# Optimization experiments

Hardware: AMD Instinct MI355X
Metric: run time of the kernel (lower is better)

## Reference

```python
import jax, jax.numpy as jnp
import numpy as np

# Multi-scale feature pyramid (H, W) per level: strides 8/16/32/64 on a ~512px image
SHAPES = ((64, 64), (32, 32), (16, 16), (8, 8))
N_HEADS, N_LEVELS, N_POINTS = 8, 4, 4
D_MODEL = 256
HEAD_DIM = D_MODEL // N_HEADS


def setup_inputs() -> dict:
    key = jax.random.key(0)
    ks = jax.random.split(key, 11)
    B, C = 4, D_MODEL
    Lv = sum(h * w for h, w in SHAPES)  # 5440
    Lq = Lv  # encoder self-attention: queries are the flattened features
    scale = 0.02
    return {
        "query": jax.random.normal(ks[0], (B, Lq, C), jnp.float32),
        "reference_points": jax.random.uniform(ks[1], (B, Lq, N_LEVELS, 2), jnp.float32),
        "value": jax.random.normal(ks[2], (B, Lv, C), jnp.float32),
        "W_off": jax.random.normal(ks[3], (C, N_HEADS * N_LEVELS * N_POINTS * 2), jnp.float32) * scale,
        "b_off": jax.random.normal(ks[4], (N_HEADS * N_LEVELS * N_POINTS * 2,), jnp.float32) * 0.5,
        "W_attn": jax.random.normal(ks[5], (C, N_HEADS * N_LEVELS * N_POINTS), jnp.float32) * scale,
        "b_attn": jax.random.normal(ks[6], (N_HEADS * N_LEVELS * N_POINTS,), jnp.float32) * scale,
        "W_val": jax.random.normal(ks[7], (C, C), jnp.float32) * scale,
        "b_val": jax.random.normal(ks[8], (C,), jnp.float32) * scale,
        "W_out": jax.random.normal(ks[9], (C, C), jnp.float32) * scale,
        "b_out": jax.random.normal(ks[10], (C,), jnp.float32) * scale,
    }


def _bilinear_sample(val, grid, H, W):
    """Replicates F.grid_sample(mode='bilinear', padding_mode='zeros', align_corners=False).

    val:  [N, C, H, W]
    grid: [N, Lq, P, 2] in [-1, 1] (x, y order)
    returns: [N, C, Lq, P]
    """
    N, C = val.shape[0], val.shape[1]
    # unnormalize (align_corners=False)
    x = (grid[..., 0] + 1.0) * 0.5 * W - 0.5  # [N, Lq, P]
    y = (grid[..., 1] + 1.0) * 0.5 * H - 0.5
    x0 = jnp.floor(x)
    y0 = jnp.floor(y)
    wx = x - x0  # fractional parts
    wy = y - y0
    flat = val.reshape(N, C, H * W)

    def gather(xi, yi):
        valid = (xi >= 0) & (xi < W) & (yi >= 0) & (yi < H)
        xc = jnp.clip(xi, 0, W - 1).astype(jnp.int32)
        yc = jnp.clip(yi, 0, H - 1).astype(jnp.int32)
        idx = yc * W + xc  # [N, Lq, P]
        g = jax.vmap(lambda v, i: v[:, i])(flat, idx)  # [N, C, Lq, P]
        return g * valid[:, None, :, :].astype(val.dtype)

    out = (gather(x0, y0) * ((1 - wx) * (1 - wy))[:, None]
           + gather(x0 + 1, y0) * (wx * (1 - wy))[:, None]
           + gather(x0, y0 + 1) * ((1 - wx) * wy)[:, None]
           + gather(x0 + 1, y0 + 1) * (wx * wy)[:, None])
    return out


def _ms_deform_attn(query, reference_points, value, W_off, b_off, W_attn, b_attn,
                    W_val, b_val, W_out, b_out):
    B, Lq, C = query.shape
    val = value @ W_val + b_val  # [B, Lv, C]
    val = val.reshape(B, -1, N_HEADS, HEAD_DIM)

    offsets = (query @ W_off + b_off).reshape(B, Lq, N_HEADS, N_LEVELS, N_POINTS, 2)
    weights = jax.nn.softmax(
        (query @ W_attn + b_attn).reshape(B, Lq, N_HEADS, N_LEVELS * N_POINTS), axis=-1
    ).reshape(B, Lq, N_HEADS, N_LEVELS, N_POINTS)

    # offset normalizer: (W, H) per level
    offset_norm = jnp.array([[w, h] for h, w in SHAPES], jnp.float32)
    # ref_dim == 2 branch
    locs = reference_points[:, :, None, :, None, :] + offsets / offset_norm[None, None, None, :, None, :]
    grids = 2.0 * locs - 1.0  # [B, Lq, nh, nl, np, 2]

    acc = jnp.zeros((B * N_HEADS, HEAD_DIM, Lq), query.dtype)
    start = 0
    for lid, (H, W) in enumerate(SHAPES):
        # [B, HW, nh, hd] -> [B*nh, hd, H, W]
        v = val[:, start:start + H * W].transpose(0, 2, 3, 1).reshape(B * N_HEADS, HEAD_DIM, H, W)
        g = grids[:, :, :, lid].transpose(0, 2, 1, 3, 4).reshape(B * N_HEADS, Lq, N_POINTS, 2)
        s = _bilinear_sample(v, g, H, W)  # [B*nh, hd, Lq, np]
        w = weights[:, :, :, lid].transpose(0, 2, 1, 3).reshape(B * N_HEADS, 1, Lq, N_POINTS)
        acc = acc + (s * w).sum(-1)
        start += H * W

    out = acc.reshape(B, D_MODEL, Lq).transpose(0, 2, 1)  # [B, Lq, C]
    return out @ W_out + b_out


def reference(query, reference_points, value, W_off, b_off, W_attn, b_attn,
              W_val, b_val, W_out, b_out):
    return _ms_deform_attn(query, reference_points, value, W_off, b_off,
                           W_attn, b_attn, W_val, b_val, W_out, b_out)
```

## Files before the change

kernel.cpp:

```cpp
#include <hip/hip_runtime.h>


typedef __attribute__((ext_vector_type(8))) _Float16 half8;
typedef __attribute__((ext_vector_type(4))) _Float16 half4;
typedef __attribute__((ext_vector_type(4))) float f32x4;

typedef __attribute__((address_space(3))) unsigned int lds_uint;
typedef const __attribute__((address_space(1))) unsigned int g_uint;

__device__ __forceinline__ void load_lds16(const _Float16* g, _Float16* l) {
    __builtin_amdgcn_global_load_lds((g_uint*)g, (lds_uint*)l, 16, 0, 0);
}

__device__ __forceinline__ half8 splat8(_Float16 v) {
    half8 r = {v, v, v, v, v, v, v, v};
    return r;
}

#define M_TOTAL 21760

__global__ __launch_bounds__(256) void prep_w(
    const float* __restrict__ W_val, const float* __restrict__ W_off,
    const float* __restrict__ W_attn, _Float16* __restrict__ wtf)
{
    const int slot = blockIdx.x * 256 + threadIdx.x;
    const int T = slot >> 11;
    const int rem = slot & 2047;
    const int n = rem >> 5;
    const int k0 = (rem & 31) * 8;
    half8 h;
#pragma unroll
    for (int e = 0; e < 8; ++e) {
        const int k = k0 + e;
        float v;
        if (T < 4) {
            v = W_val[k * 256 + T * 64 + n];
        } else {
            const int n2 = (T - 4) * 64 + n;
            v = (n2 < 256) ? W_off[k * 256 + n2] : W_attn[k * 128 + (n2 - 256)];
        }
        h[e] = (_Float16)v;
    }
    const int dbyte = T * 32768 + n * 512 + ((k0 * 2) ^ ((n & 7) << 4));
    *(half8*)(wtf + (dbyte >> 1)) = h;
}

__global__ __launch_bounds__(256) void gemm12_cvt(
    const float* __restrict__ value, const float* __restrict__ query,
    const _Float16* __restrict__ wtf,
    const float* __restrict__ b_val, const float* __restrict__ b_off,
    const float* __restrict__ b_attn,
    _Float16* __restrict__ valh, _Float16* __restrict__ offh)
{
    __shared__ _Float16 Asw[64 * 256];
    __shared__ _Float16 Bsw[64 * 256];

    const int bid = ((int)blockIdx.x % 8) * 425 + ((int)blockIdx.x / 8);

    const bool g1 = bid < 1360;
    const int id = g1 ? bid : bid - 1360;
    const int mt = g1 ? (id >> 2) : (id / 6);
    const int nt = g1 ? (id & 3) : (id % 6);
    const int NN = g1 ? 256 : 384;
    const float* A = g1 ? value : query;
    _Float16* C = g1 ? valh : offh;
    const int bm = mt * 64;
    const int bn = nt * 64;
    const int T  = g1 ? nt : 4 + nt;

    const int tid = threadIdx.x;
    const int wave = tid >> 6, lane = tid & 63;
    const int ml = lane & 15, q = lane >> 4;

    const _Float16* wsrc = wtf + ((size_t)T << 14);
#pragma unroll
    for (int i = 0; i < 8; ++i)
        load_lds16(wsrc + (((size_t)i * 256 + tid) << 3),
                   Bsw + (((size_t)i * 256 + wave * 64) << 3));

    const int rbase = wave * 16;
    float4 pa[16];
#pragma unroll
    for (int rr = 0; rr < 16; ++rr)
        pa[rr] = *(const float4*)(A + (size_t)(bm + rbase + rr) * 256 + lane * 4);
#pragma unroll
    for (int rr = 0; rr < 16; ++rr) {
        const int row = rbase + rr;
        const float4 v = pa[rr];
        const half4 h = {(_Float16)v.x, (_Float16)v.y, (_Float16)v.z, (_Float16)v.w};
        const int wbyte = row * 512 + ((lane * 8) ^ ((row & 7) << 4));
        *(half4*)(Asw + (wbyte >> 1)) = h;
    }

    __syncthreads();

    const int swl = (ml & 7) << 4;
    const int abase = (rbase + ml) * 512;

    const f32x4 zero4 = {0.f, 0.f, 0.f, 0.f};
    f32x4 acc[4] = {zero4, zero4, zero4, zero4};

#pragma unroll
    for (int kt = 0; kt < 8; ++kt) {
        const int koff = (kt * 64 + q * 16) ^ swl;
        const half8 af = *(const half8*)(Asw + ((abase + koff) >> 1));
#pragma unroll
        for (int j = 0; j < 4; ++j) {
            const half8 bf = *(const half8*)(Bsw + ((((j * 16 + ml) * 512) + koff) >> 1));
            acc[j] = __builtin_amdgcn_mfma_f32_16x16x32_f16(af, bf, acc[j], 0, 0, 0);
        }
    }

    const int r0 = q * 4;
#pragma unroll
    for (int j = 0; j < 4; ++j) {
        const int col = bn + j * 16 + ml;
        const float bj = g1 ? b_val[col] : (col < 256 ? b_off[col] : b_attn[col - 256]);
        const size_t rbaseC = (size_t)(bm + rbase + r0) * NN + col;
#pragma unroll
        for (int r = 0; r < 4; ++r)
            C[rbaseC + (size_t)r * NN] = (_Float16)(acc[j][r] + bj);
    }
}

__device__ __forceinline__ void gemm_core(
    const _Float16* __restrict__ A, const _Float16* __restrict__ Bt,
    const float* __restrict__ bias, float* __restrict__ Cv,
    int NN, int mt, int nt)
{
    __shared__ _Float16 Ah[128 * 32];
    __shared__ _Float16 Bh[64 * 32];

    const int tid = threadIdx.x;
    const int bm = mt * 128;
    const int bn = nt * 64;
    const int wave = tid >> 6, lane = tid & 63;
    const int wm = (wave & 1) * 64, wn = (wave >> 1) * 32;
    const int ml = lane & 15, kq = (lane >> 4) * 8;
    const int lr = lane >> 2;
    const int lk = (lane & 3) * 8;

    const f32x4 zero4 = {0.f, 0.f, 0.f, 0.f};
    f32x4 acc[4][2];
#pragma unroll
    for (int i = 0; i < 4; ++i)
#pragma unroll
        for (int j = 0; j < 2; ++j) acc[i][j] = zero4;

    for (int kt = 0; kt < 8; ++kt) {
        const int k0 = kt * 32;
        __syncthreads();
#pragma unroll
        for (int t = 0; t < 2; ++t) {
            const int row = wave * 32 + t * 16;
            load_lds16(A + (size_t)(bm + row + lr) * 256 + k0 + lk,
                       Ah + (size_t)row * 32);
        }
        {
            const int row = wave * 16;
            load_lds16(Bt + (size_t)(bn + row + lr) * 256 + k0 + lk,
                       Bh + (size_t)row * 32);
        }
        __syncthreads();

        half8 af[4], bf[2];
#pragma unroll
        for (int i = 0; i < 4; ++i)
            af[i] = *(const half8*)(Ah + (wm + i * 16 + ml) * 32 + kq);
#pragma unroll
        for (int j = 0; j < 2; ++j)
            bf[j] = *(const half8*)(Bh + (wn + j * 16 + ml) * 32 + kq);
#pragma unroll
        for (int i = 0; i < 4; ++i)
#pragma unroll
            for (int j = 0; j < 2; ++j)
                acc[i][j] = __builtin_amdgcn_mfma_f32_16x16x32_f16(af[i], bf[j], acc[i][j], 0, 0, 0);
    }

    const int r0 = (lane >> 4) * 4;
#pragma unroll
    for (int j = 0; j < 2; ++j) {
        const int col = bn + wn + j * 16 + ml;
        const float bj = bias[col];
#pragma unroll
        for (int i = 0; i < 4; ++i) {
            const size_t rbase = (size_t)(bm + wm + i * 16 + r0) * NN + col;
#pragma unroll
            for (int r = 0; r < 4; ++r)
                Cv[rbase + (size_t)r * NN] = acc[i][j][r] + bj;
        }
    }
}

__global__ __launch_bounds__(256) void gemm_single(
    const _Float16* __restrict__ A, const _Float16* __restrict__ Bt,
    const float* __restrict__ bias, float* __restrict__ Cv)
{
    const int id = blockIdx.x;
    gemm_core(A, Bt, bias, Cv, 256, id >> 2, id & 3);
}

__global__ __launch_bounds__(256, 4) void sample_f16(
    const _Float16* __restrict__ valh,
    const float* __restrict__ refp,
    const _Float16* __restrict__ offh,
    const float* __restrict__ W_out,
    _Float16* __restrict__ wto,
    _Float16* __restrict__ acc_out)
{
    if (blockIdx.x < 256)
        wto[blockIdx.x * 256 + threadIdx.x] =
            (_Float16)W_out[threadIdx.x * 256 + blockIdx.x];

    const int wave = threadIdx.x >> 6, lane = threadIdx.x & 63;
    const int q2 = lane >> 5, sl = lane & 31;
    const int bq = blockIdx.x * 8 + wave * 2 + q2;
    const int b = bq / 5440;
    const int h = sl >> 2;
    const int t = sl & 3;
    const int d8 = t * 8;

    const int Wt = 64 >> t;
    const float fW = (float)Wt;

    const half8 ofr = *(const half8*)(offh + (size_t)bq * 384 + h * 32 + t * 8);
    const half4 lgt = *(const half4*)(offh + (size_t)bq * 384 + 256 + h * 16 + t * 4);
    const float2 rxy = *(const float2*)(refp + (size_t)bq * 8 + t * 2);

    float lg[4];
#pragma unroll
    for (int p = 0; p < 4; ++p) lg[p] = (float)lgt[p];

    float mx = fmaxf(fmaxf(lg[0], lg[1]), fmaxf(lg[2], lg[3]));
    mx = fmaxf(mx, __shfl_xor(mx, 1));
    mx = fmaxf(mx, __shfl_xor(mx, 2));
    float s = 0.f;
#pragma unroll
    for (int p = 0; p < 4; ++p) { lg[p] = __expf(lg[p] - mx); s += lg[p]; }
    s += __shfl_xor(s, 1);
    s += __shfl_xor(s, 2);
    const float inv = 1.f / s;

    unsigned pk[16];
#pragma unroll
    for (int p = 0; p < 4; ++p) {
        const float aw = lg[p] * inv;
        const float ox = (float)ofr[p * 2];
        const float oy = (float)ofr[p * 2 + 1];
        const float x = fmaf(rxy.x, fW, ox) - 0.5f;
        const float y = fmaf(rxy.y, fW, oy) - 0.5f;
        const float x0f = floorf(x), y0f = floorf(y);
        const int x0 = (int)x0f, y0 = (int)y0f;
        const float wx = x - x0f, wy = y - y0f;
        const bool okx0 = ((unsigned)x0 < (unsigned)Wt);
        const bool okx1 = ((unsigned)(x0 + 1) < (unsigned)Wt);
        const bool oky0 = ((unsigned)y0 < (unsigned)Wt);
        const bool oky1 = ((unsigned)(y0 + 1) < (unsigned)Wt);
        const int xc0 = min(max(x0, 0), Wt - 1);
        const int xc1 = min(max(x0 + 1, 0), Wt - 1);
        const int yc0 = min(max(y0, 0), Wt - 1);
        const int yc1 = min(max(y0 + 1, 0), Wt - 1);
        const _Float16 w0 = (_Float16)((okx0 & oky0) ? (1.f - wx) * (1.f - wy) * aw : 0.f);
        const _Float16 w1 = (_Float16)((okx1 & oky0) ? wx * (1.f - wy) * aw : 0.f);
        const _Float16 w2 = (_Float16)((okx0 & oky1) ? (1.f - wx) * wy * aw : 0.f);
        const _Float16 w3 = (_Float16)((okx1 & oky1) ? wx * wy * aw : 0.f);
        pk[p * 4 + 0] = ((unsigned)(yc0 * Wt + xc0) << 16) |
                        (unsigned)__builtin_bit_cast(unsigned short, w0);
        pk[p * 4 + 1] = ((unsigned)(yc0 * Wt + xc1) << 16) |
                        (unsigned)__builtin_bit_cast(unsigned short, w1);
        pk[p * 4 + 2] = ((unsigned)(yc1 * Wt + xc0) << 16) |
                        (unsigned)__builtin_bit_cast(unsigned short, w2);
        pk[p * 4 + 3] = ((unsigned)(yc1 * Wt + xc1) << 16) |
                        (unsigned)__builtin_bit_cast(unsigned short, w3);
    }

    const int starts_[4] = {0, 4096, 5120, 5376};
    const int gbase = lane & ~3;

    half8 acc = splat8((_Float16)0.f);
#pragma unroll
    for (int l = 0; l < 4; ++l) {
        const _Float16* vbase = valh + ((size_t)(b * 5440 + starts_[l])) * 256 + h * 32 + d8;
        const int src = gbase + l;

        unsigned q_[16];
#pragma unroll
        for (int c = 0; c < 16; ++c)
            q_[c] = (unsigned)__shfl((int)pk[c], src);

        __builtin_amdgcn_sched_barrier(0);
        half8 c_[16];
#pragma unroll
        for (int c = 0; c < 16; ++c)
            c_[c] = *(const half8*)(vbase + ((size_t)(q_[c] >> 16) << 8));
        __builtin_amdgcn_sched_barrier(0);
#pragma unroll
        for (int c = 0; c < 16; ++c)
            acc += c_[c] * splat8(__builtin_bit_cast(_Float16, (unsigned short)(q_[c] & 0xffffu)));
    }

    *(half8*)(acc_out + (size_t)bq * 256 + h * 32 + d8) = acc;
}

extern "C" void kernel_launch(void* const* d_in, const int* in_sizes, int n_in,
                              void* d_out, int out_size, void* d_ws, size_t ws_size,
                              hipStream_t stream) {
    const float* query  = (const float*)d_in[0];
    const float* refp   = (const float*)d_in[1];
    const float* value  = (const float*)d_in[2];
    const float* W_off  = (const float*)d_in[3];
    const float* b_off  = (const float*)d_in[4];
    const float* W_attn = (const float*)d_in[5];
    const float* b_attn = (const float*)d_in[6];
    const float* W_val  = (const float*)d_in[7];
    const float* b_val  = (const float*)d_in[8];
    const float* W_out  = (const float*)d_in[9];
    const float* b_out  = (const float*)d_in[10];
    float* out = (float*)d_out;

    const size_t M = M_TOTAL;

    _Float16* valh  = (_Float16*)d_ws;
    _Float16* offh  = valh + M * 256;
    _Float16* acc16 = offh + M * 384;
    _Float16* wto   = acc16 + M * 256;
    _Float16* wtf   = wto + 256 * 256;

    dim3 blk(256);
    prep_w<<<dim3(80), blk, 0, stream>>>(W_val, W_off, W_attn, wtf);
    gemm12_cvt<<<dim3(3400), blk, 0, stream>>>(
        value, query, wtf, b_val, b_off, b_attn, valh, offh);
    sample_f16<<<dim3(M / 8), blk, 0, stream>>>(valh, refp, offh, W_out, wto, acc16);
    gemm_single<<<dim3(680), blk, 0, stream>>>(acc16, wto, b_out, out);
}
```

Baseline: 178.9 us.

## Fuse output projection GEMM into sampling kernel via LDS-staged MFMA

The sampling kernel now handles 16 queries per 512-thread block and writes its per-query attention output into a swizzled LDS tile. It then multiplies that tile by the transposed W_out with MFMA and writes the final fp32 output plus bias, so the separate output GEMM launch and the fp16 intermediate round trip through global memory go away. The W_out transpose/convert moves into the prep_w kernel. The cost is that every block rereads the full 256x256 W_out from global or L2 without LDS staging, and the new launch bounds may change occupancy of the gather-heavy sampling phase.

```diff
diff --git a/kernel.cpp b/kernel.cpp
--- a/kernel.cpp
+++ b/kernel.cpp
@@ -21,8 +21,14 @@
 
 __global__ __launch_bounds__(256) void prep_w(
     const float* __restrict__ W_val, const float* __restrict__ W_off,
-    const float* __restrict__ W_attn, _Float16* __restrict__ wtf)
+    const float* __restrict__ W_attn, const float* __restrict__ W_out,
+    _Float16* __restrict__ wtf, _Float16* __restrict__ wto)
 {
+    if (blockIdx.x >= 80) {
+        const int n = blockIdx.x - 80;
+        wto[n * 256 + threadIdx.x] = (_Float16)W_out[threadIdx.x * 256 + n];
+        return;
+    }
     const int slot = blockIdx.x * 256 + threadIdx.x;
     const int T = slot >> 11;
     const int rem = slot & 2047;
@@ -123,98 +129,21 @@
     }
 }
 
-__device__ __forceinline__ void gemm_core(
-    const _Float16* __restrict__ A, const _Float16* __restrict__ Bt,
-    const float* __restrict__ bias, float* __restrict__ Cv,
-    int NN, int mt, int nt)
-{
-    __shared__ _Float16 Ah[128 * 32];
-    __shared__ _Float16 Bh[64 * 32];
-
-    const int tid = threadIdx.x;
-    const int bm = mt * 128;
-    const int bn = nt * 64;
-    const int wave = tid >> 6, lane = tid & 63;
-    const int wm = (wave & 1) * 64, wn = (wave >> 1) * 32;
-    const int ml = lane & 15, kq = (lane >> 4) * 8;
-    const int lr = lane >> 2;
-    const int lk = (lane & 3) * 8;
-
-    const f32x4 zero4 = {0.f, 0.f, 0.f, 0.f};
-    f32x4 acc[4][2];
-#pragma unroll
-    for (int i = 0; i < 4; ++i)
-#pragma unroll
-        for (int j = 0; j < 2; ++j) acc[i][j] = zero4;
-
-    for (int kt = 0; kt < 8; ++kt) {
-        const int k0 = kt * 32;
-        __syncthreads();
-#pragma unroll
-        for (int t = 0; t < 2; ++t) {
-            const int row = wave * 32 + t * 16;
-            load_lds16(A + (size_t)(bm + row + lr) * 256 + k0 + lk,
-                       Ah + (size_t)row * 32);
-        }
-        {
-            const int row = wave * 16;
-            load_lds16(Bt + (size_t)(bn + row + lr) * 256 + k0 + lk,
-                       Bh + (size_t)row * 32);
-        }
-        __syncthreads();
-
-        half8 af[4], bf[2];
-#pragma unroll
-        for (int i = 0; i < 4; ++i)
-            af[i] = *(const half8*)(Ah + (wm + i * 16 + ml) * 32 + kq);
-#pragma unroll
-        for (int j = 0; j < 2; ++j)
-            bf[j] = *(const half8*)(Bh + (wn + j * 16 + ml) * 32 + kq);
-#pragma unroll
-        for (int i = 0; i < 4; ++i)
-#pragma unroll
-            for (int j = 0; j < 2; ++j)
-                acc[i][j] = __builtin_amdgcn_mfma_f32_16x16x32_f16(af[i], bf[j], acc[i][j], 0, 0, 0);
-    }
-
-    const int r0 = (lane >> 4) * 4;
-#pragma unroll
-    for (int j = 0; j < 2; ++j) {
-        const int col = bn + wn + j * 16 + ml;
-        const float bj = bias[col];
-#pragma unroll
-        for (int i = 0; i < 4; ++i) {
-            const size_t rbase = (size_t)(bm + wm + i * 16 + r0) * NN + col;
-#pragma unroll
-            for (int r = 0; r < 4; ++r)
-                Cv[rbase + (size_t)r * NN] = acc[i][j][r] + bj;
-        }
-    }
-}
-
-__global__ __launch_bounds__(256) void gemm_single(
-    const _Float16* __restrict__ A, const _Float16* __restrict__ Bt,
-    const float* __restrict__ bias, float* __restrict__ Cv)
-{
-    const int id = blockIdx.x;
-    gemm_core(A, Bt, bias, Cv, 256, id >> 2, id & 3);
-}
-
-__global__ __launch_bounds__(256, 4) void sample_f16(
+__global__ __launch_bounds__(512) void sample_out(
     const _Float16* __restrict__ valh,
     const float* __restrict__ refp,
     const _Float16* __restrict__ offh,
-    const float* __restrict__ W_out,
-    _Float16* __restrict__ wto,
-    _Float16* __restrict__ acc_out)
+    const _Float16* __restrict__ wto,
+    const float* __restrict__ b_out,
+    float* __restrict__ out)
 {
-    if (blockIdx.x < 256)
-        wto[blockIdx.x * 256 + threadIdx.x] =
-            (_Float16)W_out[threadIdx.x * 256 + blockIdx.x];
-
-    const int wave = threadIdx.x >> 6, lane = threadIdx.x & 63;
+    __shared__ _Float16 accT[16 * 256];
+
+    const int tid = threadIdx.x;
+    const int wave = tid >> 6, lane = tid & 63;
     const int q2 = lane >> 5, sl = lane & 31;
-    const int bq = blockIdx.x * 8 + wave * 2 + q2;
+    const int bql = wave * 2 + q2;
+    const int bq = blockIdx.x * 16 + bql;
     const int b = bq / 5440;
     const int h = sl >> 2;
     const int t = sl & 3;
@@ -299,7 +228,41 @@
             acc += c_[c] * splat8(__builtin_bit_cast(_Float16, (unsigned short)(q_[c] & 0xffffu)));
     }
 
-    *(half8*)(acc_out + (size_t)bq * 256 + h * 32 + d8) = acc;
+    {
+        const int cbyte = (h * 32 + d8) * 2;
+        const int wbyte = bql * 512 + (cbyte ^ ((bql & 7) << 4));
+        *(half8*)(accT + (wbyte >> 1)) = acc;
+    }
+    __syncthreads();
+
+    const int ml = lane & 15, q = lane >> 4;
+    const int wc0 = wave * 32;
+    const f32x4 zero4 = {0.f, 0.f, 0.f, 0.f};
+    f32x4 o[2] = {zero4, zero4};
+
+#pragma unroll
+    for (int kt = 0; kt < 8; ++kt) {
+        const int koff = kt * 64 + q * 16;
+        const half8 af = *(const half8*)(accT +
+            ((ml * 512 + (koff ^ ((ml & 7) << 4))) >> 1));
+#pragma unroll
+        for (int j = 0; j < 2; ++j) {
+            const int col = wc0 + j * 16 + ml;
+            const half8 bf = *(const half8*)(wto + (size_t)col * 256 + kt * 32 + q * 8);
+            o[j] = __builtin_amdgcn_mfma_f32_16x16x32_f16(af, bf, o[j], 0, 0, 0);
+        }
+    }
+
+    const int r0 = q * 4;
+    const size_t bq0 = (size_t)blockIdx.x * 16;
+#pragma unroll
+    for (int j = 0; j < 2; ++j) {
+        const int col = wc0 + j * 16 + ml;
+        const float bj = b_out[col];
+#pragma unroll
+        for (int r = 0; r < 4; ++r)
+            out[(bq0 + r0 + r) * 256 + col] = o[j][r] + bj;
+    }
 }
 
 extern "C" void kernel_launch(void* const* d_in, const int* in_sizes, int n_in,
@@ -322,14 +285,13 @@
 
     _Float16* valh  = (_Float16*)d_ws;
     _Float16* offh  = valh + M * 256;
-    _Float16* acc16 = offh + M * 384;
-    _Float16* wto   = acc16 + M * 256;
+    _Float16* wto   = offh + M * 384;
     _Float16* wtf   = wto + 256 * 256;
 
     dim3 blk(256);
-    prep_w<<<dim3(80), blk, 0, stream>>>(W_val, W_off, W_attn, wtf);
+    prep_w<<<dim3(336), blk, 0, stream>>>(W_val, W_off, W_attn, W_out, wtf, wto);
     gemm12_cvt<<<dim3(3400), blk, 0, stream>>>(
         value, query, wtf, b_val, b_off, b_attn, valh, offh);
-    sample_f16<<<dim3(M / 8), blk, 0, stream>>>(valh, refp, offh, W_out, wto, acc16);
-    gemm_single<<<dim3(680), blk, 0, stream>>>(acc16, wto, b_out, out);
-}
+    sample_out<<<dim3(M / 16), dim3(512), 0, stream>>>(
+        valh, refp, offh, wto, b_out, out);
+}
```

New measurement: 189.4 us. 1.06x slower.
